# Kernel tuning notes

Hardware: AMD Instinct MI355X
Metric: run time of the kernel (lower is better)

The kernel has to match this reference:

```python
import jax, jax.numpy as jnp
import numpy as np

EPS = 1e-6

def _ln(x):
    m = jnp.mean(x, axis=-1, keepdims=True)
    v = jnp.mean((x - m) ** 2, axis=-1, keepdims=True)
    return (x - m) * jax.lax.rsqrt(v + EPS)

def _quant(x):
    # dynamic per-token symmetric int8 quant (fused_kernels.quant_sum semantics)
    s = jnp.maximum(jnp.max(jnp.abs(x), axis=-1, keepdims=True) / 127.0, 1e-8)
    q = jnp.clip(jnp.round(x / s), -127.0, 127.0)
    return q, s, jnp.sum(q, axis=-1, keepdims=True)

def _w8a8(x, qw, sw, zw, b):
    # W8A8OF16LinearDynamicInputScale: int8 GEMM + zero-point correction via row sum
    q, s, qsum = _quant(x)
    acc = q @ qw.astype(jnp.float32).T - qsum * zw.astype(jnp.float32)
    return acc * (s * sw) + b

def _self_attn(xm, Wqkv, bqkv, Wo, bo, H):
    Bt, S, C = xm.shape
    hd = C // H
    qkv = (xm @ Wqkv.T + bqkv).reshape(Bt, S, 3, H, hd)
    q, k, v = qkv[:, :, 0], qkv[:, :, 1], qkv[:, :, 2]
    attn = jnp.einsum('bqhd,bkhd->bhqk', q * (hd ** -0.5), k).astype(jnp.float32)
    attn = jax.nn.softmax(attn, axis=-1)
    out = jnp.einsum('bhqk,bkhd->bqhd', attn, v).reshape(Bt, S, C)
    return out @ Wo.T + bo

def _cross_attn(x, y, qw_q, sw_q, zw_q, b_q, Wkv, bkv, qw_cp, sw_cp, zw_cp, b_cp, H):
    B, N, C = x.shape
    hd = C // H
    q = _w8a8(x, qw_q, sw_q, zw_q, b_q).reshape(B * N, H, hd)
    kv = (y.reshape(-1, C) @ Wkv.T + bkv).reshape(-1, 2, H, hd)
    k, v = kv[:, 0], kv[:, 1]
    # mask=None path: q (1,B*N,H,hd) attends over all B*M keys (flattened)
    attn = jnp.einsum('qhd,khd->hqk', q * (hd ** -0.5), k).astype(jnp.float32)
    attn = jax.nn.softmax(attn, axis=-1)
    out = jnp.einsum('hqk,khd->qhd', attn, v).reshape(B, N, C)
    return _w8a8(out, qw_cp, sw_cp, zw_cp, b_cp)

def setup_inputs() -> dict:
    key = jax.random.key(0)
    ks = iter(jax.random.split(key, 32))
    B, T, S, C, H, M = 2, 8, 256, 1152, 16, 224
    Dh = int(C * 4.0)
    r = lambda shape, sc=1.0: jax.random.normal(next(ks), shape, dtype=jnp.float32) * sc
    qi = lambda shape: jax.random.randint(next(ks), shape, -127, 128, dtype=jnp.int8)
    zi = lambda shape: jax.random.randint(next(ks), shape, -8, 9, dtype=jnp.int32)
    su = lambda shape: jax.random.uniform(next(ks), shape, minval=0.005, maxval=0.02, dtype=jnp.float32)
    return dict(
        x=r((B, T * S, C)), y=r((B, M, C)), t=r((B, 6 * C)),
        sst=r((6, C), C ** -0.5),
        Wqkv=r((3 * C, C), 0.02), bqkv=r((3 * C,), 0.02),
        Wo=r((C, C), 0.02), bo=r((C,), 0.02),
        Wkv=r((2 * C, C), 0.02), bkv=r((2 * C,), 0.02),
        qw_q=qi((C, C)), sw_q=su((C,)), zw_q=zi((C,)), b_q=r((C,), 0.02),
        qw_cp=qi((C, C)), sw_cp=su((C,)), zw_cp=zi((C,)), b_cp=r((C,), 0.02),
        qw_f1=qi((Dh, C)), sw_f1=su((Dh,)), zw_f1=zi((Dh,)), b_f1=r((Dh,), 0.02),
        qw_f2=qi((C, Dh)), sw_f2=su((C,)), zw_f2=zi((C,)), b_f2=r((C,), 0.02),
        num_heads=H, T=T, S=S,
    )

def reference(x, y, t, sst, Wqkv, bqkv, Wo, bo, Wkv, bkv,
              qw_q, sw_q, zw_q, b_q, qw_cp, sw_cp, zw_cp, b_cp,
              qw_f1, sw_f1, zw_f1, b_f1, qw_f2, sw_f2, zw_f2, b_f2,
              num_heads, T, S):
    B, N, C = x.shape
    mod = sst[None] + t.reshape(B, 6, C)  # (B,6,C)
    shift_msa, scale_msa, gate_msa, shift_mlp, scale_mlp, gate_mlp = (
        mod[:, 0:1], mod[:, 1:2], mod[:, 2:3], mod[:, 3:4], mod[:, 4:5], mod[:, 5:6])
    # --- self-attention (spatial, temporal=False): B (T S) C -> (B T) S C ---
    x_m = _ln(x) * (1.0 + scale_msa) + shift_msa
    x_m = x_m.reshape(B * T, S, C)
    x_m = _self_attn(x_m, Wqkv, bqkv, Wo, bo, num_heads).reshape(B, N, C)
    x = x + gate_msa * x_m  # fused_kernels.gate_residual
    # --- int8 cross-attention ---
    x = x + _cross_attn(x, y, qw_q, sw_q, zw_q, b_q, Wkv, bkv, qw_cp, sw_cp, zw_cp, b_cp, num_heads)
    # --- int8 MLP with fused gelu_quant_sum (tanh-approx GELU) ---
    x_m = _ln(x) * (1.0 + scale_mlp) + shift_mlp
    h = _w8a8(x_m, qw_f1, sw_f1, zw_f1, b_f1)
    h = jax.nn.gelu(h, approximate=True)
    h = _w8a8(h, qw_f2, sw_f2, zw_f2, b_f2)
    x = x + gate_mlp * h
    return x
```

## Files before the change

### kernel.cpp

```cpp
#include <hip/hip_runtime.h>
#include <stdint.h>

typedef unsigned short u16;
typedef _Float16 f16;
typedef f16    f16v8  __attribute__((ext_vector_type(8)));
typedef u16    u16v8  __attribute__((ext_vector_type(8)));
typedef float  f32x4  __attribute__((ext_vector_type(4)));
typedef int    i32x4  __attribute__((ext_vector_type(4)));
typedef int    i32x16 __attribute__((ext_vector_type(16)));

#define MFMA_F16(a,b,c)   __builtin_amdgcn_mfma_f32_16x16x32_f16((a),(b),(c),0,0,0)
#define MFMA_I8_32(a,b,c) __builtin_amdgcn_mfma_i32_32x32x32_i8((a),(b),(c),0,0,0)

__device__ __forceinline__ float b2f(u16 u){ union{unsigned u;float f;}v; v.u=((unsigned)u)<<16; return v.f; }
__device__ __forceinline__ u16 f2b(float f){ union{float f;unsigned u;}v; v.f=f;
  return (u16)((v.u + 0x7fffu + ((v.u>>16)&1u))>>16); }
__device__ __forceinline__ u16 f2h(float f){ f16 h = (f16)f; return __builtin_bit_cast(u16, h); }
__device__ __forceinline__ float h2f(u16 u){ return (float)__builtin_bit_cast(f16, u); }
__device__ __forceinline__ f16v8 ldh8(const u16* p){ return __builtin_bit_cast(f16v8, *(const u16v8*)p); }
__device__ __forceinline__ void gl2lds16(const void* g, void* l){
  __builtin_amdgcn_global_load_lds(
    (const __attribute__((address_space(1))) unsigned int*)g,
    (__attribute__((address_space(3))) unsigned int*)l,
    16, 0, 0);
}
__device__ __forceinline__ float gelu_t(float x){
  float t = tanhf(0.7978845608028654f*(x + 0.044715f*x*x*x));
  return 0.5f*x*(1.0f+t);
}

__global__ void mod_add_k(const float* __restrict__ sst, const float* __restrict__ t, float* __restrict__ mod){
  int i = blockIdx.x*256 + threadIdx.x;
  if (i < 2*6*1152) mod[i] = sst[i % 6912] + t[i];
}
__global__ void split2h_k(const float* __restrict__ src, u16* __restrict__ hi, u16* __restrict__ lo, int n){
  int i = blockIdx.x*256 + threadIdx.x;
  if (i >= n) return;
  float v = src[i];
  f16 h = (f16)v;
  hi[i] = __builtin_bit_cast(u16, h);
  lo[i] = f2h(v - (float)h);
}
__global__ void cross_prep_k(const int* __restrict__ qw_q, int8_t* __restrict__ w8q,
                             const int* __restrict__ qw_cp, int8_t* __restrict__ w8cp,
                             const float* __restrict__ Wkv, u16* __restrict__ wkvh, u16* __restrict__ wkvl,
                             const float* __restrict__ y, u16* __restrict__ yf){
  const int S1 = 1327104, S2 = 2654208, S3 = 5308416, S4 = 5824512;
  int i = blockIdx.x*256 + threadIdx.x;
  if (i < S1){ w8q[i] = (int8_t)qw_q[i]; }
  else if (i < S2){ int j = i - S1; w8cp[j] = (int8_t)qw_cp[j]; }
  else if (i < S3){ int j = i - S2; float v = Wkv[j]; f16 h = (f16)v;
    wkvh[j] = __builtin_bit_cast(u16, h); wkvl[j] = f2h(v - (float)h); }
  else if (i < S4){ int j = i - S3; yf[j] = f2h(y[j]); }
}
__global__ void mlp_prep_k(const int* __restrict__ qw_f1, int8_t* __restrict__ w8f1,
                           const int* __restrict__ qw_f2, int8_t* __restrict__ w8f2){
  const int S1 = 5308416, S2 = 10616832;
  int i = blockIdx.x*256 + threadIdx.x;
  if (i < S1){ w8f1[i] = (int8_t)qw_f1[i]; }
  else if (i < S2){ int j = i - S1; w8f2[j] = (int8_t)qw_f2[j]; }
}
__global__ void ln_mod_f16_k(const float* __restrict__ src, u16* __restrict__ xf,
                             const float* __restrict__ mod, int shift_row, int scale_row){
  const int row = blockIdx.x, tid = threadIdx.x;
  const int b = row >> 11;
  const float* ms = mod + ((size_t)b*6 + shift_row)*1152;
  const float* mc = mod + ((size_t)b*6 + scale_row)*1152;
  __shared__ float r1[256], r2[256];
  float s = 0.f, sq = 0.f, vals[5]; int cnt = 0;
  for (int c = tid; c < 1152; c += 256){
    float v = src[(size_t)row*1152+c];
    vals[cnt++] = v; s += v; sq += v*v;
  }
  r1[tid]=s; r2[tid]=sq; __syncthreads();
  for (int st=128; st>0; st>>=1){ if (tid<st){ r1[tid]+=r1[tid+st]; r2[tid]+=r2[tid+st]; } __syncthreads(); }
  float mean = r1[0]*(1.f/1152.f);
  float var  = r2[0]*(1.f/1152.f) - mean*mean;
  float rstd = rsqrtf(var + 1e-6f);
  cnt = 0;
  for (int c = tid; c < 1152; c += 256){
    float v = (vals[cnt++]-mean)*rstd*(1.f+mc[c]) + ms[c];
    xf[(size_t)row*1152+c] = f2h(v);
  }
}
__global__ void rgq_k(const float* __restrict__ x, const float* __restrict__ ao,
                      const float* __restrict__ mod, int gate_row, float* __restrict__ xw,
                      int8_t* __restrict__ q8, float* __restrict__ s_out, int* __restrict__ q_out){
  const int row = blockIdx.x, tid = threadIdx.x;
  const int b = row >> 11;
  const float* mg = mod + ((size_t)b*6 + gate_row)*1152;
  __shared__ float r1[256];
  __shared__ int ri[256];
  float mx = 0.f, vals[5]; int cnt = 0;
  for (int c = tid; c < 1152; c += 256){
    float v = x[(size_t)row*1152+c] + mg[c]*ao[(size_t)row*1152+c];
    xw[(size_t)row*1152+c] = v;
    vals[cnt++] = v; mx = fmaxf(mx, fabsf(v));
  }
  r1[tid]=mx; __syncthreads();
  for (int st=128; st>0; st>>=1){ if (tid<st) r1[tid]=fmaxf(r1[tid],r1[tid+st]); __syncthreads(); }
  const float s_ = fmaxf(r1[0]*(1.f/127.f), 1e-8f);
  const float inv = 1.f/s_;
  int acc = 0; cnt = 0;
  for (int c = tid; c < 1152; c += 256){
    float q = rintf(vals[cnt++]*inv);
    q = fminf(fmaxf(q, -127.f), 127.f);
    q8[(size_t)row*1152+c] = (int8_t)q;
    acc += (int)q;
  }
  ri[tid]=acc; __syncthreads();
  for (int st=128; st>0; st>>=1){ if (tid<st) ri[tid]+=ri[tid+st]; __syncthreads(); }
  if (tid==0){ s_out[row]=s_; q_out[row]=ri[0]; }
}
__global__ void rlq_k(float* __restrict__ xw, const float* __restrict__ add,
                      const float* __restrict__ mod, int shift_row, int scale_row,
                      int8_t* __restrict__ q8, float* __restrict__ s_out, int* __restrict__ q_out){
  const int row = blockIdx.x, tid = threadIdx.x;
  const int b = row >> 11;
  const float* ms = mod + ((size_t)b*6 + shift_row)*1152;
  const float* mc = mod + ((size_t)b*6 + scale_row)*1152;
  __shared__ float r1[256], r2[256];
  __shared__ int ri[256];
  float s = 0.f, sq = 0.f, vals[5]; int cnt = 0;
  for (int c = tid; c < 1152; c += 256){
    float v = xw[(size_t)row*1152+c] + add[(size_t)row*1152+c];
    xw[(size_t)row*1152+c] = v;
    vals[cnt++] = v; s += v; sq += v*v;
  }
  r1[tid]=s; r2[tid]=sq; __syncthreads();
  for (int st=128; st>0; st>>=1){ if (tid<st){ r1[tid]+=r1[tid+st]; r2[tid]+=r2[tid+st]; } __syncthreads(); }
  float mean = r1[0]*(1.f/1152.f);
  float var  = r2[0]*(1.f/1152.f) - mean*mean;
  float rstd = rsqrtf(var + 1e-6f);
  __syncthreads();
  float mx = 0.f; cnt = 0;
  for (int c = tid; c < 1152; c += 256){
    float v = (vals[cnt]-mean)*rstd*(1.f+mc[c]) + ms[c];
    vals[cnt++] = v; mx = fmaxf(mx, fabsf(v));
  }
  r1[tid]=mx; __syncthreads();
  for (int st=128; st>0; st>>=1){ if (tid<st) r1[tid]=fmaxf(r1[tid],r1[tid+st]); __syncthreads(); }
  const float s_ = fmaxf(r1[0]*(1.f/127.f), 1e-8f);
  const float inv = 1.f/s_;
  int acc = 0; cnt = 0;
  for (int c = tid; c < 1152; c += 256){
    float q = rintf(vals[cnt++]*inv);
    q = fminf(fmaxf(q, -127.f), 127.f);
    q8[(size_t)row*1152+c] = (int8_t)q;
    acc += (int)q;
  }
  ri[tid]=acc; __syncthreads();
  for (int st=128; st>0; st>>=1){ if (tid<st) ri[tid]+=ri[tid+st]; __syncthreads(); }
  if (tid==0){ s_out[row]=s_; q_out[row]=ri[0]; }
}
template<int SRC_F32>
__global__ void quant_rows_k(const void* __restrict__ src, int C_,
                             int8_t* __restrict__ q8, float* __restrict__ s_out, int* __restrict__ q_out){
  const int row = blockIdx.x, tid = threadIdx.x;
  __shared__ float red[256];
  __shared__ int redi[256];
  float vals[18];
  float mx = 0.f; int cnt = 0;
  for (int c = tid; c < C_; c += 256){
    float v = SRC_F32 ? ((const float*)src)[(size_t)row*C_+c] : b2f(((const u16*)src)[(size_t)row*C_+c]);
    vals[cnt++] = v;
    mx = fmaxf(mx, fabsf(v));
  }
  red[tid]=mx; __syncthreads();
  for (int st=128; st>0; st>>=1){ if (tid<st) red[tid]=fmaxf(red[tid],red[tid+st]); __syncthreads(); }
  const float s_ = fmaxf(red[0]*(1.f/127.f), 1e-8f);
  const float inv = 1.f/s_;
  int acc = 0; cnt = 0;
  for (int c = tid; c < C_; c += 256){
    float q = rintf(vals[cnt++]*inv);
    q = fminf(fmaxf(q, -127.f), 127.f);
    q8[(size_t)row*C_+c] = (int8_t)q;
    acc += (int)q;
  }
  redi[tid]=acc; __syncthreads();
  for (int st=128; st>0; st>>=1){ if (tid<st) redi[tid]+=redi[tid+st]; __syncthreads(); }
  if (tid==0){ s_out[row]=s_; q_out[row]=redi[0]; }
}

template<int MODE>
__global__ __launch_bounds__(256,4) void gemm_f16k(
    const u16* __restrict__ Af, int lda,
    const u16* __restrict__ Wh, const u16* __restrict__ Wl, int ldw,
    const float* __restrict__ bias, float* __restrict__ out, int ldo, int M, int K,
    u16* __restrict__ e1, u16* __restrict__ e2){
  __shared__ u16 sA[128*32];
  __shared__ u16 sWh[128*32];
  __shared__ u16 sWl[128*32];
  const int tid = threadIdx.x, lane = tid & 63;
  const int wv = tid >> 6, wx = wv & 1, wy = wv >> 1;
  const int quad = lane >> 4, l16 = lane & 15;
  const int m0 = blockIdx.y*128, n0 = blockIdx.x*128;
  f32x4 acc[4][4];
  #pragma unroll
  for (int i=0;i<4;i++)
    #pragma unroll
    for (int j=0;j<4;j++) acc[i][j] = (f32x4){0.f,0.f,0.f,0.f};
  for (int k0=0; k0<K; k0+=32){
    #pragma unroll
    for (int r=0;r<2;r++){
      int slotbase = r*256 + wv*64;
      int slot = slotbase + lane;
      int row = slot >> 2;
      int col8 = ((slot ^ (row>>1)) & 3) * 8;
      int gm = m0 + row; if (gm > M-1) gm = M-1;
      size_t aoff = (size_t)gm*lda + k0 + col8;
      size_t woff = (size_t)(n0+row)*ldw + k0 + col8;
      gl2lds16(Af + aoff, &sA[(size_t)slotbase*8]);
      gl2lds16(Wh + woff, &sWh[(size_t)slotbase*8]);
      gl2lds16(Wl + woff, &sWl[(size_t)slotbase*8]);
    }
    __syncthreads();
    const int cs = ((quad ^ ((l16>>1)&3)) * 8);
    f16v8 a[4], bh[4], bl[4];
    #pragma unroll
    for (int i=0;i<4;i++) a[i] = ldh8(&sA[(wy*64+i*16+l16)*32 + cs]);
    #pragma unroll
    for (int j=0;j<4;j++){
      bh[j] = ldh8(&sWh[(wx*64+j*16+l16)*32 + cs]);
      bl[j] = ldh8(&sWl[(wx*64+j*16+l16)*32 + cs]);
    }
    #pragma unroll
    for (int i=0;i<4;i++)
      #pragma unroll
      for (int j=0;j<4;j++){
        acc[i][j] = MFMA_F16(a[i], bh[j], acc[i][j]);
        acc[i][j] = MFMA_F16(a[i], bl[j], acc[i][j]);
      }
    __syncthreads();
  }
  #pragma unroll
  for (int j=0;j<4;j++){
    int col = n0 + wx*64 + j*16 + l16;
    float bc = bias ? bias[col] : 0.f;
    #pragma unroll
    for (int i=0;i<4;i++)
      #pragma unroll
      for (int r=0;r<4;r++){
        int row = m0 + wy*64 + i*16 + quad*4 + r;
        if (row >= M) continue;
        float v = acc[i][j][r] + bc;
        if (MODE == 0){
          out[(size_t)row*ldo + col] = v;
        } else if (MODE == 1){
          if (col < 2304){
            e1[(size_t)row*2304 + col] = f2h(v);
          } else {
            int vc = col - 2304;
            int hd_ = vc/72, d = vc - hd_*72;
            int z = row >> 8, s2 = row & 255;
            e2[((size_t)(z*16+hd_)*80 + d)*256 + s2] = f2h(v);
          }
        } else {
          if (col < 1152){
            e1[(size_t)row*1152 + col] = f2h(v);
          } else {
            int vc = col - 1152;
            int hd_ = vc/72, d = vc - hd_*72;
            e2[((size_t)hd_*80 + d)*448 + row] = f2h(v);
          }
        }
      }
  }
}

__global__ __launch_bounds__(256,3) void gemm_i8(
    const int8_t* __restrict__ A, int lda, const int8_t* __restrict__ W, int ldw,
    const float* __restrict__ rs, const int* __restrict__ rq,
    const float* __restrict__ sw, const int* __restrict__ zw, const float* __restrict__ bias,
    void* __restrict__ out, int ldo, int M, int K, int do_gelu, int out_f32,
    const float* __restrict__ xwf, const float* __restrict__ modf, int do_final){
  __shared__ int8_t As[128*128];
  __shared__ int8_t Bs[128*128];
  const int tid = threadIdx.x, lane = tid & 63, wv = tid >> 6;
  const int wx = wv & 1, wy = wv >> 1;
  const int l32 = lane & 31, g = lane >> 5;
  const int m0 = blockIdx.y*128, n0 = blockIdx.x*128;
  const int srow = lane >> 3, schunk = lane & 7;
  const int scol = ((schunk ^ srow) & 7) * 16;
  i32x16 acc[2][2];
  #pragma unroll
  for (int i=0;i<2;i++)
    #pragma unroll
    for (int j=0;j<2;j++)
      #pragma unroll
      for (int r=0;r<16;r++) acc[i][j][r] = 0;
  for (int k0 = 0; k0 < K; k0 += 128){
    #pragma unroll
    for (int i=0;i<4;i++){
      int rr = (i*4 + wv)*8;
      int gm = m0 + rr + srow; if (gm > M-1) gm = M-1;
      gl2lds16(A + (size_t)gm*lda + k0 + scol, &As[rr*128]);
      int gn = n0 + rr + srow;
      gl2lds16(W + (size_t)gn*ldw + k0 + scol, &Bs[rr*128]);
    }
    __syncthreads();
    #pragma unroll
    for (int kq=0; kq<4; kq++){
      i32x4 af[2], bw[2];
      #pragma unroll
      for (int i=0;i<2;i++){
        int row = wy*64 + i*32 + l32;
        int cs = (((kq*2 + g) ^ (row & 7))) * 16;
        af[i] = *(const i32x4*)&As[row*128 + cs];
      }
      #pragma unroll
      for (int j=0;j<2;j++){
        int row = wx*64 + j*32 + l32;
        int cs = (((kq*2 + g) ^ (row & 7))) * 16;
        bw[j] = *(const i32x4*)&Bs[row*128 + cs];
      }
      #pragma unroll
      for (int i=0;i<2;i++)
        #pragma unroll
        for (int j=0;j<2;j++)
          acc[i][j] = MFMA_I8_32(af[i], bw[j], acc[i][j]);
    }
    __syncthreads();
  }
  #pragma unroll
  for (int j=0;j<2;j++){
    int col = n0 + wx*64 + j*32 + l32;
    float swc = sw[col]; float zwc = (float)zw[col]; float bc = bias[col];
    #pragma unroll
    for (int i=0;i<2;i++)
      #pragma unroll
      for (int r=0;r<16;r++){
        int row = m0 + wy*64 + i*32 + (r&3) + 8*(r>>2) + 4*g;
        if (row < M){
          float v = ((float)acc[i][j][r] - (float)rq[row]*zwc) * (rs[row]*swc) + bc;
          if (do_gelu) v = gelu_t(v);
          if (do_final){
            int bb = row >> 11;
            float ov = xwf[(size_t)row*1152 + col] + modf[((size_t)bb*6+5)*1152 + col]*v;
            ((float*)out)[(size_t)row*ldo + col] = ov;
          } else if (out_f32) ((float*)out)[(size_t)row*ldo + col] = v;
          else                ((u16*)out)[(size_t)row*ldo + col] = f2b(v);
        }
      }
  }
}

__global__ __launch_bounds__(256) void attn_self_f16(
    const u16* __restrict__ qkf, const u16* __restrict__ vtf,
    u16* __restrict__ of, float scale){
  constexpr int NT = 16, PSTR = 264, VSTR = 256;
  __shared__ u16 P[4*16*PSTR];
  const int tid = threadIdx.x, lane = tid & 63, wv = tid >> 6;
  const int quad = lane >> 4, l16 = lane & 15;
  const int h = blockIdx.y, z = blockIdx.z;
  const int qbase = z*256 + blockIdx.x*64;
  const u16* Vth = vtf + (size_t)(z*16+h)*80*VSTR;
  const f16v8 zf = __builtin_bit_cast(f16v8, (u16v8)0);
  const int mrow = qbase + wv*16 + l16;

  f16v8 qf[3];
  #pragma unroll
  for (int t=0;t<3;t++){
    if (t==2 && quad!=0){ qf[t]=zf; }
    else qf[t] = ldh8(qkf + (size_t)mrow*2304 + h*72 + t*32 + (t==2?0:quad*8));
  }
  f32x4 sc[NT];
  #pragma unroll
  for (int nt=0; nt<NT; nt++){
    f32x4 a = {0.f,0.f,0.f,0.f};
    #pragma unroll
    for (int t=0;t<3;t++){
      f16v8 kf = zf;
      if (!(t==2 && quad!=0))
        kf = ldh8(qkf + (size_t)(z*256 + nt*16 + l16)*2304 + 1152 + h*72 + t*32 + (t==2?0:quad*8));
      a = MFMA_F16(qf[t], kf, a);
    }
    sc[nt] = a;
  }
  float mx[4] = {-1e30f,-1e30f,-1e30f,-1e30f};
  #pragma unroll
  for (int nt=0; nt<NT; nt++)
    #pragma unroll
    for (int r=0;r<4;r++){ float v = sc[nt][r]*scale; sc[nt][r]=v; mx[r]=fmaxf(mx[r],v); }
  #pragma unroll
  for (int r=0;r<4;r++)
    for (int d=1; d<16; d<<=1) mx[r] = fmaxf(mx[r], __shfl_xor(mx[r], d, 64));
  float sm[4] = {0.f,0.f,0.f,0.f};
  #pragma unroll
  for (int nt=0; nt<NT; nt++)
    #pragma unroll
    for (int r=0;r<4;r++){ float p = __expf(sc[nt][r]-mx[r]); sc[nt][r]=p; sm[r]+=p; }
  #pragma unroll
  for (int r=0;r<4;r++){
    for (int d=1; d<16; d<<=1) sm[r] += __shfl_xor(sm[r], d, 64);
    sm[r] = 1.f/sm[r];
  }
  u16* Pw = P + wv*16*PSTR;
  #pragma unroll
  for (int nt=0; nt<NT; nt++)
    #pragma unroll
    for (int r=0;r<4;r++)
      Pw[(quad*4+r)*PSTR + nt*16 + l16] = f2h(sc[nt][r]*sm[r]);
  const u16* Pr = P + wv*16*PSTR + (size_t)l16*PSTR;
  #pragma unroll
  for (int dt=0; dt<5; dt++){
    f32x4 o = {0.f,0.f,0.f,0.f};
    #pragma unroll
    for (int kk=0; kk<8; kk++){
      f16v8 pv = ldh8(Pr + kk*32 + quad*8);
      f16v8 bv = ldh8(Vth + (size_t)(dt*16+l16)*VSTR + kk*32 + quad*8);
      o = MFMA_F16(pv, bv, o);
    }
    int d = dt*16 + l16;
    if (d < 72){
      #pragma unroll
      for (int r=0;r<4;r++){
        int row = qbase + wv*16 + quad*4 + r;
        of[(size_t)row*1152 + h*72 + d] = f2h(o[r]);
      }
    }
  }
}

__global__ __launch_bounds__(256) void attn_cross_f16(
    const float* __restrict__ Q32,
    const u16* __restrict__ Kf,
    const u16* __restrict__ Vt,
    float* __restrict__ O, float scale){
  constexpr int NT = 28, PSTR = 456, VSTR = 448;
  __shared__ u16 P[4*16*PSTR];
  const int tid = threadIdx.x, lane = tid & 63, wv = tid >> 6;
  const int quad = lane >> 4, l16 = lane & 15;
  const int h = blockIdx.y;
  const int qbase = blockIdx.x*64;
  const u16* Vth = Vt + (size_t)h*80*VSTR;
  const f16v8 zf = __builtin_bit_cast(f16v8, (u16v8)0);

  const int mrow = qbase + wv*16 + l16;
  const float* qp = Q32 + (size_t)mrow*1152 + h*72;
  f16v8 qf[3];
  #pragma unroll
  for (int t=0;t<3;t++){
    if (t==2 && quad!=0){ qf[t]=zf; continue; }
    u16v8 hv;
    #pragma unroll
    for (int j=0;j<8;j++) hv[j] = f2h(qp[t*32 + (t==2?0:quad*8) + j]);
    qf[t] = __builtin_bit_cast(f16v8, hv);
  }
  f32x4 sc[NT];
  #pragma unroll
  for (int nt=0; nt<NT; nt++){
    f32x4 a = {0.f,0.f,0.f,0.f};
    #pragma unroll
    for (int t=0;t<3;t++){
      f16v8 kf = zf;
      if (!(t==2 && quad!=0))
        kf = ldh8(Kf + (size_t)(nt*16 + l16)*1152 + h*72 + t*32 + (t==2?0:quad*8));
      a = MFMA_F16(qf[t], kf, a);
    }
    sc[nt] = a;
  }
  float mx[4] = {-1e30f,-1e30f,-1e30f,-1e30f};
  #pragma unroll
  for (int nt=0; nt<NT; nt++)
    #pragma unroll
    for (int r=0;r<4;r++){ float v = sc[nt][r]*scale; sc[nt][r]=v; mx[r]=fmaxf(mx[r],v); }
  #pragma unroll
  for (int r=0;r<4;r++)
    for (int d=1; d<16; d<<=1) mx[r] = fmaxf(mx[r], __shfl_xor(mx[r], d, 64));
  float sm[4] = {0.f,0.f,0.f,0.f};
  #pragma unroll
  for (int nt=0; nt<NT; nt++)
    #pragma unroll
    for (int r=0;r<4;r++){ float p = __expf(sc[nt][r]-mx[r]); sc[nt][r]=p; sm[r]+=p; }
  #pragma unroll
  for (int r=0;r<4;r++){
    for (int d=1; d<16; d<<=1) sm[r] += __shfl_xor(sm[r], d, 64);
    sm[r] = 1.f/sm[r];
  }
  u16* Pw = P + wv*16*PSTR;
  #pragma unroll
  for (int nt=0; nt<NT; nt++)
    #pragma unroll
    for (int r=0;r<4;r++)
      Pw[(quad*4+r)*PSTR + nt*16 + l16] = f2h(sc[nt][r]*sm[r]);
  const u16* Pr = P + wv*16*PSTR + (size_t)l16*PSTR;
  #pragma unroll
  for (int dt=0; dt<5; dt++){
    f32x4 o = {0.f,0.f,0.f,0.f};
    #pragma unroll
    for (int kk=0; kk<14; kk++){
      f16v8 pv = ldh8(Pr + kk*32 + quad*8);
      f16v8 bv = ldh8(Vth + (size_t)(dt*16+l16)*VSTR + kk*32 + quad*8);
      o = MFMA_F16(pv, bv, o);
    }
    int d = dt*16 + l16;
    if (d < 72){
      #pragma unroll
      for (int r=0;r<4;r++){
        int row = qbase + wv*16 + quad*4 + r;
        O[(size_t)row*1152 + h*72 + d] = o[r];
      }
    }
  }
}

extern "C" void kernel_launch(void* const* d_in, const int* in_sizes, int n_in,
                              void* d_out, int out_size, void* d_ws, size_t ws_size,
                              hipStream_t stream){
  const float* x    = (const float*)d_in[0];
  const float* y    = (const float*)d_in[1];
  const float* t    = (const float*)d_in[2];
  const float* sst  = (const float*)d_in[3];
  const float* Wqkv = (const float*)d_in[4];
  const float* bqkv = (const float*)d_in[5];
  const float* Wo   = (const float*)d_in[6];
  const float* bo   = (const float*)d_in[7];
  const float* Wkv  = (const float*)d_in[8];
  const float* bkv  = (const float*)d_in[9];
  const int*   qw_q  = (const int*)d_in[10];
  const float* sw_q  = (const float*)d_in[11];
  const int*   zw_q  = (const int*)d_in[12];
  const float* b_q   = (const float*)d_in[13];
  const int*   qw_cp = (const int*)d_in[14];
  const float* sw_cp = (const float*)d_in[15];
  const int*   zw_cp = (const int*)d_in[16];
  const float* b_cp  = (const float*)d_in[17];
  const int*   qw_f1 = (const int*)d_in[18];
  const float* sw_f1 = (const float*)d_in[19];
  const int*   zw_f1 = (const int*)d_in[20];
  const float* b_f1  = (const float*)d_in[21];
  const int*   qw_f2 = (const int*)d_in[22];
  const float* sw_f2 = (const float*)d_in[23];
  const int*   zw_f2 = (const int*)d_in[24];
  const float* b_f2  = (const float*)d_in[25];
  (void)in_sizes; (void)n_in; (void)out_size;

  constexpr size_t SZR = (size_t)4096*1152*4;
  constexpr size_t R0 = 0;
  constexpr size_t R1 = R0 + SZR;
  constexpr size_t R2 = R1 + SZR;
  constexpr size_t R3 = R2 + SZR;
  constexpr size_t R4 = R3 + SZR;
  constexpr size_t R5 = R4 + (size_t)9437184;
  constexpr size_t R6 = R5 + (size_t)9437184;
  constexpr size_t RS = R6 + (size_t)10485760;
  constexpr size_t RQ = RS + (size_t)4096*4;
  constexpr size_t RM = RQ + (size_t)4096*4;
  constexpr size_t WS_NEED = RM + (size_t)2*6*1152*4;
  if (ws_size < WS_NEED) return;

  char* ws = (char*)d_ws;
  float*  xw    = (float*)(ws + R0);
  u16*    wqkvh = (u16*)(ws + R1);
  u16*    wqkvl = (u16*)(ws + R1 + (size_t)3456*1152*2);
  u16*    wkvh  = (u16*)(ws + R1);
  u16*    wkvl  = (u16*)(ws + R1 + (size_t)2304*1152*2);
  u16*    yf    = (u16*)(ws + R1 + (size_t)2*2304*1152*2);
  float*  q32   = (float*)(ws + R1);
  float*  cpout = (float*)(ws + R1);
  int8_t* q8h   = (int8_t*)(ws + R1);
  u16*    qkf   = (u16*)(ws + R2);
  float*  aof   = (float*)(ws + R2);
  u16*    hbuf  = (u16*)(ws + R2);
  u16*    xmf   = (u16*)(ws + R4);
  u16*    of    = (u16*)(ws + R4);
  u16*    kf    = (u16*)(ws + R4 + (size_t)4128768);
  u16*    vtc   = (u16*)(ws + R4 + (size_t)6193152);
  int8_t* w8f2  = (int8_t*)(ws + R4);
  int8_t* w8q   = (int8_t*)(ws + R5);
  int8_t* w8cp  = (int8_t*)(ws + R5 + (size_t)1327104);
  int8_t* w8f1  = (int8_t*)(ws + R5 + (size_t)2654208);
  u16*    vtf   = (u16*)(ws + R6);
  u16*    woh   = (u16*)(ws + R6);
  u16*    wol   = (u16*)(ws + R6 + (size_t)1152*1152*2);
  int8_t* q8x   = (int8_t*)(ws + R6);
  float*  rs    = (float*)(ws + RS);
  int*    rq    = (int*)(ws + RQ);
  float*  mod   = (float*)(ws + RM);

  const float scale = 0.11785113019775793f;

  mod_add_k<<<(2*6*1152+255)/256,256,0,stream>>>(sst, t, mod);

  ln_mod_f16_k<<<4096,256,0,stream>>>(x, xmf, mod, 0, 1);
  split2h_k<<<(3456*1152+255)/256,256,0,stream>>>(Wqkv, wqkvh, wqkvl, 3456*1152);
  gemm_f16k<1><<<dim3(27,32),256,0,stream>>>(xmf,1152, wqkvh,wqkvl,1152, bqkv, nullptr,0, 4096,1152, qkf,vtf);
  attn_self_f16<<<dim3(4,16,16),256,0,stream>>>(qkf, vtf, of, scale);
  split2h_k<<<(1152*1152+255)/256,256,0,stream>>>(Wo, woh, wol, 1152*1152);
  gemm_f16k<0><<<dim3(9,32),256,0,stream>>>(of,1152, woh,wol,1152, bo, aof,1152, 4096,1152, nullptr,nullptr);
  rgq_k<<<4096,256,0,stream>>>(x, aof, mod, 2, xw, q8x, rs, rq);

  cross_prep_k<<<(5824512+255)/256,256,0,stream>>>(qw_q,w8q, qw_cp,w8cp, Wkv,wkvh,wkvl, y,yf);
  gemm_f16k<2><<<dim3(18,4),256,0,stream>>>(yf,1152, wkvh,wkvl,1152, bkv, nullptr,0, 448,1152, kf,vtc);
  gemm_i8<<<dim3(9,32),256,0,stream>>>(q8x,1152, w8q,1152, rs,rq, sw_q,zw_q,b_q, q32,1152, 4096,1152, 0, 1, nullptr,nullptr,0);
  attn_cross_f16<<<dim3(64,16),256,0,stream>>>(q32, kf, vtc, aof, scale);
  quant_rows_k<1><<<4096,256,0,stream>>>(aof, 1152, q8x, rs, rq);
  gemm_i8<<<dim3(9,32),256,0,stream>>>(q8x,1152, w8cp,1152, rs,rq, sw_cp,zw_cp,b_cp, cpout,1152, 4096,1152, 0, 1, nullptr,nullptr,0);

  rlq_k<<<4096,256,0,stream>>>(xw, cpout, mod, 3, 4, q8x, rs, rq);
  mlp_prep_k<<<(10616832+255)/256,256,0,stream>>>(qw_f1, w8f1, qw_f2, w8f2);
  gemm_i8<<<dim3(36,32),256,0,stream>>>(q8x,1152, w8f1,1152, rs,rq, sw_f1,zw_f1,b_f1, hbuf,4608, 4096,1152, 1, 0, nullptr,nullptr,0);
  quant_rows_k<0><<<4096,256,0,stream>>>(hbuf, 4608, q8h, rs, rq);
  gemm_i8<<<dim3(9,32),256,0,stream>>>(q8h,4608, w8f2,4608, rs,rq, sw_f2,zw_f2,b_f2, d_out,1152, 4096,4608, 0, 1, xw,mod,1);
}
```

Baseline: 815.4 us.

## Add 256x256-tile triple-buffered QKV GEMM with phased MFMA/load interleave

Replaces the generic f16 split-weight GEMM for the QKV projection with a dedicated kernel. It uses 512 threads, 256x256 output tiles, three LDS buffers of 48 KB each filled by direct global-to-LDS loads, and four sub-phases per k-step that interleave prefetch with MFMA work under raised wave priority. Blocks are remapped in groups of 8 to improve L2 reuse. The larger tiles cut redundant global traffic and raise MFMA density, at the cost of 144 KB of dynamic LDS, a grid of only 224 blocks, and a column clamp that wastes work on padded tiles.

After: 791.5 us. 1.03x faster.

```diff
diff --git a/kernel.cpp b/kernel.cpp
--- a/kernel.cpp
+++ b/kernel.cpp
@@ -266,6 +266,144 @@
         }
       }
   }
+}
+
+#define QKV_NT 36
+__global__ __launch_bounds__(512,2) void gemm_qkv_8ph(
+    const u16* __restrict__ Af,
+    const u16* __restrict__ Wh_, const u16* __restrict__ Wl_,
+    const float* __restrict__ bias,
+    u16* __restrict__ qkf, u16* __restrict__ vtf){
+  extern __shared__ u16 sm[];
+  char* smb = (char*)sm;
+  const int tid = threadIdx.x, lane = tid & 63, wv = tid >> 6;
+  const int wr = wv >> 2, wc = wv & 3;
+  const int quad = lane >> 4, l16 = lane & 15;
+  const int c = blockIdx.x & 7, bi = blockIdx.x >> 3;
+  const int m0 = (((c>>1)<<2) + (bi&3)) << 8;
+  const int n0 = ((c&1)*7 + (bi>>2)) << 8;
+
+  const u16* gA[2]; const u16* gH[2]; const u16* gL[2];
+  int sbase[2];
+  #pragma unroll
+  for (int r=0;r<2;r++){
+    int slot = r*512 + tid;
+    int row = slot >> 2;
+    int col8 = ((slot ^ (row>>1)) & 3) * 8;
+    sbase[r] = (r*512 + wv*64) * 16;
+    gA[r] = Af + (size_t)(m0+row)*1152 + col8;
+    int gn = n0 + row; if (gn > 3455) gn = 3455;
+    gH[r] = Wh_ + (size_t)gn*1152 + col8;
+    gL[r] = Wl_ + (size_t)gn*1152 + col8;
+  }
+
+  #define STG_A(t2,b) { size_t ko=(size_t)(t2)*32; \
+    gl2lds16(gA[0]+ko, smb + (b)*49152 + sbase[0]); \
+    gl2lds16(gA[1]+ko, smb + (b)*49152 + sbase[1]); }
+  #define STG_H(t2,b) { size_t ko=(size_t)(t2)*32; \
+    gl2lds16(gH[0]+ko, smb + (b)*49152 + 16384 + sbase[0]); \
+    gl2lds16(gH[1]+ko, smb + (b)*49152 + 16384 + sbase[1]); }
+  #define STG_L(t2,b) { size_t ko=(size_t)(t2)*32; \
+    gl2lds16(gL[0]+ko, smb + (b)*49152 + 32768 + sbase[0]); \
+    gl2lds16(gL[1]+ko, smb + (b)*49152 + 32768 + sbase[1]); }
+
+  STG_A(0,0); STG_H(0,0); STG_L(0,0);
+  STG_A(1,1); STG_H(1,1); STG_L(1,1);
+
+  const int cs = (quad ^ ((l16>>1)&3)) * 8;
+  const int arow = wr*128 + l16;
+  const int wrow = wc*64 + l16;
+
+  f32x4 acc[8][4];
+  #pragma unroll
+  for (int i=0;i<8;i++)
+    #pragma unroll
+    for (int j=0;j<4;j++) acc[i][j] = (f32x4){0.f,0.f,0.f,0.f};
+
+  f16v8 bh[4], bl[4];
+
+  #define PHASE(p, STAGE_STMT) { \
+    const u16* bA = sm + cur*24576; \
+    f16v8 a0 = ldh8(bA + (arow + (2*(p))*16)*32 + cs); \
+    f16v8 a1 = ldh8(bA + (arow + (2*(p)+1)*16)*32 + cs); \
+    if ((p)==0){ \
+      const u16* bH = bA + 8192; \
+      const u16* bL = bA + 16384; \
+      _Pragma("unroll") \
+      for (int j=0;j<4;j++){ \
+        bh[j] = ldh8(bH + (wrow + j*16)*32 + cs); \
+        bl[j] = ldh8(bL + (wrow + j*16)*32 + cs); \
+      } \
+    } \
+    STAGE_STMT; \
+    __builtin_amdgcn_s_barrier(); \
+    asm volatile("s_waitcnt lgkmcnt(0)" ::: "memory"); \
+    __builtin_amdgcn_sched_barrier(0); \
+    __builtin_amdgcn_s_setprio(1); \
+    _Pragma("unroll") \
+    for (int j=0;j<4;j++){ \
+      acc[2*(p)][j]   = MFMA_F16(a0, bh[j], acc[2*(p)][j]); \
+      acc[2*(p)][j]   = MFMA_F16(a0, bl[j], acc[2*(p)][j]); \
+      acc[2*(p)+1][j] = MFMA_F16(a1, bh[j], acc[2*(p)+1][j]); \
+      acc[2*(p)+1][j] = MFMA_F16(a1, bl[j], acc[2*(p)+1][j]); \
+    } \
+    __builtin_amdgcn_s_setprio(0); \
+    __builtin_amdgcn_s_barrier(); \
+  }
+
+  int cur = 0;
+  for (int t = 0; t < QKV_NT-1; ++t){
+    const int nxt = (cur == 0) ? 2 : cur - 1;
+    asm volatile("s_waitcnt vmcnt(6)" ::: "memory");
+    __builtin_amdgcn_s_barrier();
+    __builtin_amdgcn_sched_barrier(0);
+    const bool pf = (t < QKV_NT-2);
+    PHASE(0, if (pf) STG_A(t+2,nxt));
+    PHASE(1, if (pf) STG_H(t+2,nxt));
+    PHASE(2, if (pf) STG_L(t+2,nxt));
+    PHASE(3, );
+    cur = (cur == 2) ? 0 : cur + 1;
+  }
+  asm volatile("s_waitcnt vmcnt(0)" ::: "memory");
+  __builtin_amdgcn_s_barrier();
+  __builtin_amdgcn_sched_barrier(0);
+  PHASE(0, );
+  PHASE(1, );
+  PHASE(2, );
+  PHASE(3, );
+
+  #pragma unroll
+  for (int j=0;j<4;j++){
+    const int col = n0 + wc*64 + j*16 + l16;
+    if (col < 3456){
+      const float bc = bias[col];
+      if (col < 2304){
+        #pragma unroll
+        for (int i=0;i<8;i++){
+          const size_t rb = (size_t)(m0 + wr*128 + i*16 + quad*4)*2304 + col;
+          #pragma unroll
+          for (int r=0;r<4;r++)
+            qkf[rb + (size_t)r*2304] = f2h(acc[i][j][r] + bc);
+        }
+      } else {
+        const int vc = col - 2304;
+        const int hd_ = vc/72, d = vc - hd_*72;
+        #pragma unroll
+        for (int i=0;i<8;i++){
+          #pragma unroll
+          for (int r=0;r<4;r++){
+            const int row = m0 + wr*128 + i*16 + quad*4 + r;
+            const int z = row >> 8, s2 = row & 255;
+            vtf[((size_t)(z*16+hd_)*80 + d)*256 + s2] = f2h(acc[i][j][r] + bc);
+          }
+        }
+      }
+    }
+  }
+  #undef PHASE
+  #undef STG_A
+  #undef STG_H
+  #undef STG_L
 }
 
 __global__ __launch_bounds__(256,3) void gemm_i8(
@@ -581,11 +719,18 @@
 
   const float scale = 0.11785113019775793f;
 
+  static bool attr_set = false;
+  if (!attr_set){
+    hipFuncSetAttribute(reinterpret_cast<const void*>(gemm_qkv_8ph),
+                        hipFuncAttributeMaxDynamicSharedMemorySize, 3*49152);
+    attr_set = true;
+  }
+
   mod_add_k<<<(2*6*1152+255)/256,256,0,stream>>>(sst, t, mod);
 
   ln_mod_f16_k<<<4096,256,0,stream>>>(x, xmf, mod, 0, 1);
   split2h_k<<<(3456*1152+255)/256,256,0,stream>>>(Wqkv, wqkvh, wqkvl, 3456*1152);
-  gemm_f16k<1><<<dim3(27,32),256,0,stream>>>(xmf,1152, wqkvh,wqkvl,1152, bqkv, nullptr,0, 4096,1152, qkf,vtf);
+  gemm_qkv_8ph<<<dim3(224),dim3(512),3*49152,stream>>>(xmf, wqkvh, wqkvl, bqkv, qkf, vtf);
   attn_self_f16<<<dim3(4,16,16),256,0,stream>>>(qkf, vtf, of, scale);
   split2h_k<<<(1152*1152+255)/256,256,0,stream>>>(Wo, woh, wol, 1152*1152);
   gemm_f16k<0><<<dim3(9,32),256,0,stream>>>(of,1152, woh,wol,1152, bo, aof,1152, 4096,1152, nullptr,nullptr);
```
